# Optimization experiments

Hardware: AMD Instinct MI355X
Metric: run time of the kernel (lower is better)

Reference implementation:

```python
import jax, jax.numpy as jnp
import numpy as np

N_NODES = 8192
DIM = 512

def setup_inputs() -> dict:
    key = jax.random.key(0)
    k1, k2, k3, k4 = jax.random.split(key, 4)
    x = jax.random.normal(k1, (N_NODES, DIM), dtype=jnp.float32)
    adj = jax.random.uniform(k2, (N_NODES, N_NODES), dtype=jnp.float32)
    # nn.Linear(dim, dim): weight [out, in], bias [out]
    bound = 1.0 / np.sqrt(DIM)
    W = jax.random.uniform(k3, (DIM, DIM), minval=-bound, maxval=bound, dtype=jnp.float32)
    b = jax.random.uniform(k4, (DIM,), minval=-bound, maxval=bound, dtype=jnp.float32)
    return {"x": x, "adj": adj, "W": W, "b": b}

def reference(x, adj, W, b):
    # agg = adj @ x : [N, dim]
    agg = jnp.matmul(adj, x)
    # Linear: agg @ W.T + b, then ReLU
    out = jnp.matmul(agg, W.T) + b
    return jax.nn.relu(out)
```

## Files before the change

### kernel.cpp

```cpp
#include <hip/hip_runtime.h>
#include <stdint.h>

typedef __bf16 bf16_t;
typedef bf16_t bf16x8 __attribute__((ext_vector_type(8)));
typedef bf16_t bf16x4 __attribute__((ext_vector_type(4)));
typedef float f32x4 __attribute__((ext_vector_type(4)));

#define N_NODES 8192
#define DIM 512

typedef __attribute__((address_space(1))) void as1_void;
typedef __attribute__((address_space(3))) void as3_void;

__device__ __forceinline__ void gload_lds16(const void* g, void* l) {
  __builtin_amdgcn_global_load_lds((as1_void*)g, (as3_void*)l, 16, 0, 0);
}

__global__ __launch_bounds__(256) void k_transpose_x(const float* __restrict__ x,
                                                     bf16_t* __restrict__ xT) {
  __shared__ float tile[64][65];
  const int m0 = blockIdx.x * 64;
  const int n0 = blockIdx.y * 64;
  const int t = threadIdx.x;
  const int r = t >> 4;
  const int c = (t & 15) << 2;
#pragma unroll
  for (int i = 0; i < 4; ++i) {
    f32x4 v = *(const f32x4*)&x[(size_t)(m0 + r + i * 16) * DIM + n0 + c];
    tile[r + i * 16][c + 0] = v.x;
    tile[r + i * 16][c + 1] = v.y;
    tile[r + i * 16][c + 2] = v.z;
    tile[r + i * 16][c + 3] = v.w;
  }
  __syncthreads();
#pragma unroll
  for (int i = 0; i < 4; ++i) {
    const int rn = r + i * 16;
    bf16x4 o = {(bf16_t)tile[c + 0][rn], (bf16_t)tile[c + 1][rn],
                (bf16_t)tile[c + 2][rn], (bf16_t)tile[c + 3][rn]};
    *(bf16x4*)&xT[(size_t)(n0 + rn) * N_NODES + m0 + c] = o;
  }
}

__global__ __launch_bounds__(256) void k_cvt_w(const float* __restrict__ W,
                                               bf16_t* __restrict__ Wb) {
  const int t = blockIdx.x * 256 + threadIdx.x;
  f32x4 v = *(const f32x4*)&W[(size_t)t * 4];
  bf16x4 o = {(bf16_t)v.x, (bf16_t)v.y, (bf16_t)v.z, (bf16_t)v.w};
  *(bf16x4*)&Wb[(size_t)t * 4] = o;
}

template <int S>
__global__ __launch_bounds__(256, 3) void k_gemm1(const float* __restrict__ A,
                                                  const bf16_t* __restrict__ Bt,
                                                  float* __restrict__ P) {
  constexpr int K = N_NODES;
  constexpr int KC = K / S;
  constexpr int NIT = KC / 32;
  __shared__ float As[2][128 * 32];
  __shared__ bf16_t Bs[2][128 * 32];

  const int b = blockIdx.x;
  const int xcd = b & 7;
  const int i6 = b >> 3;
  const int n_tile = i6 & 3;
  const int s = (i6 >> 2) & (S - 1);
  const int mg = (i6 >> 2) / S;
  const int m0 = (mg * 8 + xcd) * 128;
  const int n0 = n_tile * 128;

  const int t = threadIdx.x;
  const int lane = t & 63;
  const int w = t >> 6;
  const int wr = w & 1;
  const int wc = w >> 1;
  const int lrow = lane & 15;
  const int quad = lane >> 4;

  const int aoff = ((t & 7) ^ ((t >> 3) & 7)) * 4;
  const int boff = ((t & 3) ^ ((t >> 3) & 3)) * 8;
  const float* ag = A + (size_t)(m0 + (t >> 3)) * K + (size_t)s * KC + aoff;
  const bf16_t* bg = Bt + (size_t)(n0 + (t >> 2)) * K + (size_t)s * KC + boff;

  auto stage = [&](int it, int buf) {
    const int kc = it * 32;
#pragma unroll
    for (int i = 0; i < 4; ++i)
      gload_lds16(ag + (size_t)(i * 32) * K + kc, &As[buf][(i * 256 + t) * 4]);
#pragma unroll
    for (int i = 0; i < 2; ++i)
      gload_lds16(bg + (size_t)(i * 64) * K + kc, &Bs[buf][(i * 256 + t) * 8]);
  };

  const int apc0 = ((quad * 2) ^ (lrow & 7)) * 4;
  const int apc1 = (((quad * 2) ^ (lrow & 7)) ^ 1) * 4;
  const int bpc = (quad ^ ((lrow >> 1) & 3)) * 8;

  f32x4 acc[4][4] = {};

  auto compute = [&](int buf) {
    bf16x8 af[4], bfr[4];
#pragma unroll
    for (int ii = 0; ii < 4; ++ii) {
      const int rb = (wr * 64 + ii * 16 + lrow) * 32;
      f32x4 a0 = *(const f32x4*)&As[buf][rb + apc0];
      f32x4 a1 = *(const f32x4*)&As[buf][rb + apc1];
#pragma unroll
      for (int z = 0; z < 4; ++z) {
        af[ii][z] = (bf16_t)a0[z];
        af[ii][z + 4] = (bf16_t)a1[z];
      }
    }
#pragma unroll
    for (int jj = 0; jj < 4; ++jj)
      bfr[jj] = *(const bf16x8*)&Bs[buf][(wc * 64 + jj * 16 + lrow) * 32 + bpc];
#pragma unroll
    for (int ii = 0; ii < 4; ++ii)
#pragma unroll
      for (int jj = 0; jj < 4; ++jj)
        acc[ii][jj] =
            __builtin_amdgcn_mfma_f32_16x16x32_bf16(af[ii], bfr[jj], acc[ii][jj], 0, 0, 0);
  };

  stage(0, 0);
  __syncthreads();
#pragma unroll 1
  for (int it = 0; it < NIT; it += 2) {
    stage(it + 1, 1);
    compute(0);
    __syncthreads();
    if (it + 2 < NIT) stage(it + 2, 0);
    compute(1);
    __syncthreads();
  }

  float* Pp = P + (size_t)s * N_NODES * DIM;
#pragma unroll
  for (int ii = 0; ii < 4; ++ii)
#pragma unroll
    for (int jj = 0; jj < 4; ++jj) {
      const int col = n0 + wc * 64 + jj * 16 + lrow;
#pragma unroll
      for (int r = 0; r < 4; ++r) {
        const int row = m0 + wr * 64 + ii * 16 + quad * 4 + r;
        Pp[(size_t)row * DIM + col] = acc[ii][jj][r];
      }
    }
}

template <int S>
__global__ __launch_bounds__(256, 2) void k_gemm2(const float* __restrict__ P,
                                                  const bf16_t* __restrict__ Bw,
                                                  const float* __restrict__ bias,
                                                  float* __restrict__ out) {
  constexpr int K = DIM;
  constexpr int LDA = 72;
  constexpr int LDB = 72;
  constexpr size_t PS = (size_t)N_NODES * DIM;
  __shared__ bf16_t As[64 * LDA];
  __shared__ bf16_t Bs[128 * LDB];

  const int b = blockIdx.x;
  const int xcd = b & 7;
  const int j = b >> 3;
  const int n0 = (j & 3) * 128;
  const int m0 = ((j >> 2) * 8 + xcd) * 64;
  const int t = threadIdx.x;
  const int lane = t & 63;
  const int w = t >> 6;
  const int wr = w & 1;
  const int wc = w >> 1;
  const int lrow = lane & 15;
  const int quad = lane >> 4;
  const int ar = t >> 2, aq = t & 3;
  const int br = t >> 1, bq = t & 1;

  const float* ap = P + (size_t)(m0 + ar) * K + aq * 16;
  const bf16_t* bp = Bw + (size_t)(n0 + br) * K + bq * 32;
  bf16_t* aw = &As[ar * LDA + aq * 16];
  bf16_t* bw = &Bs[br * LDB + bq * 32];

  f32x4 acc[2][4] = {};

  for (int k0 = 0; k0 < K; k0 += 64) {
    f32x4 av[4];
#pragma unroll
    for (int z = 0; z < 4; ++z) av[z] = *(const f32x4*)(ap + k0 + z * 4);
#pragma unroll
    for (int s2 = 1; s2 < S; ++s2)
#pragma unroll
      for (int z = 0; z < 4; ++z) av[z] += *(const f32x4*)(ap + s2 * PS + k0 + z * 4);
    bf16x8 b0 = *(const bf16x8*)(bp + k0);
    bf16x8 b1 = *(const bf16x8*)(bp + k0 + 8);
    bf16x8 b2 = *(const bf16x8*)(bp + k0 + 16);
    bf16x8 b3 = *(const bf16x8*)(bp + k0 + 24);
    bf16x8 a0, a1;
#pragma unroll
    for (int z = 0; z < 4; ++z) {
      a0[z] = (bf16_t)av[0][z];
      a0[z + 4] = (bf16_t)av[1][z];
      a1[z] = (bf16_t)av[2][z];
      a1[z + 4] = (bf16_t)av[3][z];
    }
    __syncthreads();
    *(bf16x8*)aw = a0;
    *(bf16x8*)(aw + 8) = a1;
    *(bf16x8*)bw = b0;
    *(bf16x8*)(bw + 8) = b1;
    *(bf16x8*)(bw + 16) = b2;
    *(bf16x8*)(bw + 24) = b3;
    __syncthreads();
#pragma unroll
    for (int kk = 0; kk < 64; kk += 32) {
      bf16x8 af0 = *(const bf16x8*)&As[(wr * 32 + 0 + lrow) * LDA + kk + quad * 8];
      bf16x8 af1 = *(const bf16x8*)&As[(wr * 32 + 16 + lrow) * LDA + kk + quad * 8];
      bf16x8 bf0 = *(const bf16x8*)&Bs[(wc * 64 + 0 + lrow) * LDB + kk + quad * 8];
      bf16x8 bf1 = *(const bf16x8*)&Bs[(wc * 64 + 16 + lrow) * LDB + kk + quad * 8];
      bf16x8 bf2 = *(const bf16x8*)&Bs[(wc * 64 + 32 + lrow) * LDB + kk + quad * 8];
      bf16x8 bf3 = *(const bf16x8*)&Bs[(wc * 64 + 48 + lrow) * LDB + kk + quad * 8];
      acc[0][0] = __builtin_amdgcn_mfma_f32_16x16x32_bf16(af0, bf0, acc[0][0], 0, 0, 0);
      acc[0][1] = __builtin_amdgcn_mfma_f32_16x16x32_bf16(af0, bf1, acc[0][1], 0, 0, 0);
      acc[0][2] = __builtin_amdgcn_mfma_f32_16x16x32_bf16(af0, bf2, acc[0][2], 0, 0, 0);
      acc[0][3] = __builtin_amdgcn_mfma_f32_16x16x32_bf16(af0, bf3, acc[0][3], 0, 0, 0);
      acc[1][0] = __builtin_amdgcn_mfma_f32_16x16x32_bf16(af1, bf0, acc[1][0], 0, 0, 0);
      acc[1][1] = __builtin_amdgcn_mfma_f32_16x16x32_bf16(af1, bf1, acc[1][1], 0, 0, 0);
      acc[1][2] = __builtin_amdgcn_mfma_f32_16x16x32_bf16(af1, bf2, acc[1][2], 0, 0, 0);
      acc[1][3] = __builtin_amdgcn_mfma_f32_16x16x32_bf16(af1, bf3, acc[1][3], 0, 0, 0);
    }
  }

#pragma unroll
  for (int i = 0; i < 2; ++i)
#pragma unroll
    for (int j2 = 0; j2 < 4; ++j2) {
      const int col = n0 + wc * 64 + j2 * 16 + lrow;
      const float bj = bias[col];
#pragma unroll
      for (int r = 0; r < 4; ++r) {
        const int row = m0 + wr * 32 + i * 16 + quad * 4 + r;
        float v = acc[i][j2][r] + bj;
        out[(size_t)row * DIM + col] = v > 0.0f ? v : 0.0f;
      }
    }
}

extern "C" void kernel_launch(void* const* d_in, const int* in_sizes, int n_in,
                              void* d_out, int out_size, void* d_ws, size_t ws_size,
                              hipStream_t stream) {
  const float* x = (const float*)d_in[0];
  const float* adj = (const float*)d_in[1];
  const float* W = (const float*)d_in[2];
  const float* b = (const float*)d_in[3];
  float* out = (float*)d_out;

  bf16_t* xT = (bf16_t*)d_ws;
  bf16_t* Wb = xT + (size_t)DIM * N_NODES;
  float* P = (float*)(Wb + (size_t)DIM * DIM);
  const size_t base = (size_t)DIM * N_NODES * 2 + (size_t)DIM * DIM * 2;
  const size_t pslab = (size_t)N_NODES * DIM * 4;

  k_transpose_x<<<dim3(N_NODES / 64, DIM / 64), 256, 0, stream>>>(x, xT);
  k_cvt_w<<<dim3((DIM * DIM / 4) / 256), 256, 0, stream>>>(W, Wb);

  if (ws_size >= base + 4 * pslab) {
    k_gemm1<4><<<dim3(256 * 4), 256, 0, stream>>>(adj, xT, P);
    k_gemm2<4><<<dim3(512), 256, 0, stream>>>(P, Wb, b, out);
  } else {
    k_gemm1<1><<<dim3(256), 256, 0, stream>>>(adj, xT, P);
    k_gemm2<1><<<dim3(512), 256, 0, stream>>>(P, Wb, b, out);
  }
}
```

Baseline: 507.0 us.

## Reassociate to adj@(xW^T) and fuse bias+ReLU into single main GEMM

Computes Y = x·W^T first in a small GEMM, writing it transposed in bf16, then runs a single large GEMM adj·Y with bias and ReLU fused in the epilogue. This removes the split-K partial-sum buffer, the second GEMM, and the separate transpose/convert kernels. The main kernel uses 64x128 tiles with a 4-buffer software pipeline and manual vmcnt waits. It rounds the intermediate Y to bf16 rather than the aggregated features, which changes the numerics slightly.

```diff
diff --git a/kernel.cpp b/kernel.cpp
--- a/kernel.cpp
+++ b/kernel.cpp
@@ -3,7 +3,6 @@
 
 typedef __bf16 bf16_t;
 typedef bf16_t bf16x8 __attribute__((ext_vector_type(8)));
-typedef bf16_t bf16x4 __attribute__((ext_vector_type(4)));
 typedef float f32x4 __attribute__((ext_vector_type(4)));
 
 #define N_NODES 8192
@@ -16,58 +15,16 @@
   __builtin_amdgcn_global_load_lds((as1_void*)g, (as3_void*)l, 16, 0, 0);
 }
 
-__global__ __launch_bounds__(256) void k_transpose_x(const float* __restrict__ x,
-                                                     bf16_t* __restrict__ xT) {
-  __shared__ float tile[64][65];
-  const int m0 = blockIdx.x * 64;
-  const int n0 = blockIdx.y * 64;
-  const int t = threadIdx.x;
-  const int r = t >> 4;
-  const int c = (t & 15) << 2;
-#pragma unroll
-  for (int i = 0; i < 4; ++i) {
-    f32x4 v = *(const f32x4*)&x[(size_t)(m0 + r + i * 16) * DIM + n0 + c];
-    tile[r + i * 16][c + 0] = v.x;
-    tile[r + i * 16][c + 1] = v.y;
-    tile[r + i * 16][c + 2] = v.z;
-    tile[r + i * 16][c + 3] = v.w;
-  }
-  __syncthreads();
-#pragma unroll
-  for (int i = 0; i < 4; ++i) {
-    const int rn = r + i * 16;
-    bf16x4 o = {(bf16_t)tile[c + 0][rn], (bf16_t)tile[c + 1][rn],
-                (bf16_t)tile[c + 2][rn], (bf16_t)tile[c + 3][rn]};
-    *(bf16x4*)&xT[(size_t)(n0 + rn) * N_NODES + m0 + c] = o;
-  }
-}
-
-__global__ __launch_bounds__(256) void k_cvt_w(const float* __restrict__ W,
-                                               bf16_t* __restrict__ Wb) {
-  const int t = blockIdx.x * 256 + threadIdx.x;
-  f32x4 v = *(const f32x4*)&W[(size_t)t * 4];
-  bf16x4 o = {(bf16_t)v.x, (bf16_t)v.y, (bf16_t)v.z, (bf16_t)v.w};
-  *(bf16x4*)&Wb[(size_t)t * 4] = o;
-}
-
-template <int S>
-__global__ __launch_bounds__(256, 3) void k_gemm1(const float* __restrict__ A,
-                                                  const bf16_t* __restrict__ Bt,
-                                                  float* __restrict__ P) {
-  constexpr int K = N_NODES;
-  constexpr int KC = K / S;
-  constexpr int NIT = KC / 32;
+__global__ __launch_bounds__(256) void k_yw(const float* __restrict__ x,
+                                            const float* __restrict__ W,
+                                            bf16_t* __restrict__ Yt) {
+  constexpr int NIT = DIM / 32;
   __shared__ float As[2][128 * 32];
-  __shared__ bf16_t Bs[2][128 * 32];
+  __shared__ float Bs[2][128 * 32];
 
   const int b = blockIdx.x;
-  const int xcd = b & 7;
-  const int i6 = b >> 3;
-  const int n_tile = i6 & 3;
-  const int s = (i6 >> 2) & (S - 1);
-  const int mg = (i6 >> 2) / S;
-  const int m0 = (mg * 8 + xcd) * 128;
-  const int n0 = n_tile * 128;
+  const int n0 = (b & 3) * 128;
+  const int k0 = (b >> 2) * 128;
 
   const int t = threadIdx.x;
   const int lane = t & 63;
@@ -77,24 +34,22 @@
   const int lrow = lane & 15;
   const int quad = lane >> 4;
 
-  const int aoff = ((t & 7) ^ ((t >> 3) & 7)) * 4;
-  const int boff = ((t & 3) ^ ((t >> 3) & 3)) * 8;
-  const float* ag = A + (size_t)(m0 + (t >> 3)) * K + (size_t)s * KC + aoff;
-  const bf16_t* bg = Bt + (size_t)(n0 + (t >> 2)) * K + (size_t)s * KC + boff;
+  const int srow = t >> 3;
+  const int aoff = ((t & 7) ^ (srow & 7)) * 4;
+  const float* ag = W + (size_t)(n0 + srow) * DIM + aoff;
+  const float* bg = x + (size_t)(k0 + srow) * DIM + aoff;
 
   auto stage = [&](int it, int buf) {
     const int kc = it * 32;
 #pragma unroll
-    for (int i = 0; i < 4; ++i)
-      gload_lds16(ag + (size_t)(i * 32) * K + kc, &As[buf][(i * 256 + t) * 4]);
-#pragma unroll
-    for (int i = 0; i < 2; ++i)
-      gload_lds16(bg + (size_t)(i * 64) * K + kc, &Bs[buf][(i * 256 + t) * 8]);
+    for (int i = 0; i < 4; ++i) {
+      gload_lds16(ag + (size_t)(i * 32) * DIM + kc, &As[buf][(i * 256 + t) * 4]);
+      gload_lds16(bg + (size_t)(i * 32) * DIM + kc, &Bs[buf][(i * 256 + t) * 4]);
+    }
   };
 
   const int apc0 = ((quad * 2) ^ (lrow & 7)) * 4;
   const int apc1 = (((quad * 2) ^ (lrow & 7)) ^ 1) * 4;
-  const int bpc = (quad ^ ((lrow >> 1) & 3)) * 8;
 
   f32x4 acc[4][4] = {};
 
@@ -112,8 +67,16 @@
       }
     }
 #pragma unroll
-    for (int jj = 0; jj < 4; ++jj)
-      bfr[jj] = *(const bf16x8*)&Bs[buf][(wc * 64 + jj * 16 + lrow) * 32 + bpc];
+    for (int jj = 0; jj < 4; ++jj) {
+      const int rb = (wc * 64 + jj * 16 + lrow) * 32;
+      f32x4 b0 = *(const f32x4*)&Bs[buf][rb + apc0];
+      f32x4 b1 = *(const f32x4*)&Bs[buf][rb + apc1];
+#pragma unroll
+      for (int z = 0; z < 4; ++z) {
+        bfr[jj][z] = (bf16_t)b0[z];
+        bfr[jj][z + 4] = (bf16_t)b1[z];
+      }
+    }
 #pragma unroll
     for (int ii = 0; ii < 4; ++ii)
 #pragma unroll
@@ -124,47 +87,45 @@
 
   stage(0, 0);
   __syncthreads();
+  int cur = 0;
 #pragma unroll 1
-  for (int it = 0; it < NIT; it += 2) {
-    stage(it + 1, 1);
-    compute(0);
+  for (int it = 0; it < NIT; ++it) {
+    if (it + 1 < NIT) stage(it + 1, cur ^ 1);
+    compute(cur);
     __syncthreads();
-    if (it + 2 < NIT) stage(it + 2, 0);
-    compute(1);
-    __syncthreads();
+    cur ^= 1;
   }
 
-  float* Pp = P + (size_t)s * N_NODES * DIM;
 #pragma unroll
   for (int ii = 0; ii < 4; ++ii)
 #pragma unroll
     for (int jj = 0; jj < 4; ++jj) {
-      const int col = n0 + wc * 64 + jj * 16 + lrow;
+      const int col = k0 + wc * 64 + jj * 16 + lrow;
 #pragma unroll
       for (int r = 0; r < 4; ++r) {
-        const int row = m0 + wr * 64 + ii * 16 + quad * 4 + r;
-        Pp[(size_t)row * DIM + col] = acc[ii][jj][r];
-      }
-    }
-}
-
-template <int S>
-__global__ __launch_bounds__(256, 2) void k_gemm2(const float* __restrict__ P,
-                                                  const bf16_t* __restrict__ Bw,
-                                                  const float* __restrict__ bias,
-                                                  float* __restrict__ out) {
-  constexpr int K = DIM;
-  constexpr int LDA = 72;
-  constexpr int LDB = 72;
-  constexpr size_t PS = (size_t)N_NODES * DIM;
-  __shared__ bf16_t As[64 * LDA];
-  __shared__ bf16_t Bs[128 * LDB];
+        const int row = n0 + wr * 64 + ii * 16 + quad * 4 + r;
+        Yt[(size_t)row * N_NODES + col] = (bf16_t)acc[ii][jj][r];
+      }
+    }
+}
+
+__global__ __launch_bounds__(256) void k_main(const float* __restrict__ A,
+                                              const bf16_t* __restrict__ Bt,
+                                              const float* __restrict__ bias,
+                                              float* __restrict__ out) {
+  constexpr int K = N_NODES;
+  constexpr int NIT = K / 32;
+  __shared__ float As[4][64 * 32];
+  __shared__ bf16_t Bs[4][128 * 32];
 
   const int b = blockIdx.x;
   const int xcd = b & 7;
-  const int j = b >> 3;
-  const int n0 = (j & 3) * 128;
-  const int m0 = ((j >> 2) * 8 + xcd) * 64;
+  const int i6 = b >> 3;
+  const int n_tile = i6 & 3;
+  const int mg = i6 >> 2;
+  const int m0 = (mg * 8 + xcd) * 64;
+  const int n0 = n_tile * 128;
+
   const int t = threadIdx.x;
   const int lane = t & 63;
   const int w = t >> 6;
@@ -172,73 +133,84 @@
   const int wc = w >> 1;
   const int lrow = lane & 15;
   const int quad = lane >> 4;
-  const int ar = t >> 2, aq = t & 3;
-  const int br = t >> 1, bq = t & 1;
-
-  const float* ap = P + (size_t)(m0 + ar) * K + aq * 16;
-  const bf16_t* bp = Bw + (size_t)(n0 + br) * K + bq * 32;
-  bf16_t* aw = &As[ar * LDA + aq * 16];
-  bf16_t* bw = &Bs[br * LDB + bq * 32];
+
+  const int aoff = ((t & 7) ^ ((t >> 3) & 7)) * 4;
+  const int boff = ((t & 3) ^ ((t >> 3) & 3)) * 8;
+  const float* ag = A + (size_t)(m0 + (t >> 3)) * K + aoff;
+  const bf16_t* bg = Bt + (size_t)(n0 + (t >> 2)) * K + boff;
+
+  auto stage = [&](int it, int buf) {
+    const int kc = it * 32;
+#pragma unroll
+    for (int i = 0; i < 2; ++i)
+      gload_lds16(ag + (size_t)(i * 32) * K + kc, &As[buf][(i * 256 + t) * 4]);
+#pragma unroll
+    for (int i = 0; i < 2; ++i)
+      gload_lds16(bg + (size_t)(i * 64) * K + kc, &Bs[buf][(i * 256 + t) * 8]);
+  };
+
+  const int apc0 = ((quad * 2) ^ (lrow & 7)) * 4;
+  const int apc1 = (((quad * 2) ^ (lrow & 7)) ^ 1) * 4;
+  const int bpc = (quad ^ ((lrow >> 1) & 3)) * 8;
 
   f32x4 acc[2][4] = {};
 
-  for (int k0 = 0; k0 < K; k0 += 64) {
-    f32x4 av[4];
-#pragma unroll
-    for (int z = 0; z < 4; ++z) av[z] = *(const f32x4*)(ap + k0 + z * 4);
-#pragma unroll
-    for (int s2 = 1; s2 < S; ++s2)
-#pragma unroll
-      for (int z = 0; z < 4; ++z) av[z] += *(const f32x4*)(ap + s2 * PS + k0 + z * 4);
-    bf16x8 b0 = *(const bf16x8*)(bp + k0);
-    bf16x8 b1 = *(const bf16x8*)(bp + k0 + 8);
-    bf16x8 b2 = *(const bf16x8*)(bp + k0 + 16);
-    bf16x8 b3 = *(const bf16x8*)(bp + k0 + 24);
-    bf16x8 a0, a1;
-#pragma unroll
-    for (int z = 0; z < 4; ++z) {
-      a0[z] = (bf16_t)av[0][z];
-      a0[z + 4] = (bf16_t)av[1][z];
-      a1[z] = (bf16_t)av[2][z];
-      a1[z + 4] = (bf16_t)av[3][z];
-    }
-    __syncthreads();
-    *(bf16x8*)aw = a0;
-    *(bf16x8*)(aw + 8) = a1;
-    *(bf16x8*)bw = b0;
-    *(bf16x8*)(bw + 8) = b1;
-    *(bf16x8*)(bw + 16) = b2;
-    *(bf16x8*)(bw + 24) = b3;
-    __syncthreads();
-#pragma unroll
-    for (int kk = 0; kk < 64; kk += 32) {
-      bf16x8 af0 = *(const bf16x8*)&As[(wr * 32 + 0 + lrow) * LDA + kk + quad * 8];
-      bf16x8 af1 = *(const bf16x8*)&As[(wr * 32 + 16 + lrow) * LDA + kk + quad * 8];
-      bf16x8 bf0 = *(const bf16x8*)&Bs[(wc * 64 + 0 + lrow) * LDB + kk + quad * 8];
-      bf16x8 bf1 = *(const bf16x8*)&Bs[(wc * 64 + 16 + lrow) * LDB + kk + quad * 8];
-      bf16x8 bf2 = *(const bf16x8*)&Bs[(wc * 64 + 32 + lrow) * LDB + kk + quad * 8];
-      bf16x8 bf3 = *(const bf16x8*)&Bs[(wc * 64 + 48 + lrow) * LDB + kk + quad * 8];
-      acc[0][0] = __builtin_amdgcn_mfma_f32_16x16x32_bf16(af0, bf0, acc[0][0], 0, 0, 0);
-      acc[0][1] = __builtin_amdgcn_mfma_f32_16x16x32_bf16(af0, bf1, acc[0][1], 0, 0, 0);
-      acc[0][2] = __builtin_amdgcn_mfma_f32_16x16x32_bf16(af0, bf2, acc[0][2], 0, 0, 0);
-      acc[0][3] = __builtin_amdgcn_mfma_f32_16x16x32_bf16(af0, bf3, acc[0][3], 0, 0, 0);
-      acc[1][0] = __builtin_amdgcn_mfma_f32_16x16x32_bf16(af1, bf0, acc[1][0], 0, 0, 0);
-      acc[1][1] = __builtin_amdgcn_mfma_f32_16x16x32_bf16(af1, bf1, acc[1][1], 0, 0, 0);
-      acc[1][2] = __builtin_amdgcn_mfma_f32_16x16x32_bf16(af1, bf2, acc[1][2], 0, 0, 0);
-      acc[1][3] = __builtin_amdgcn_mfma_f32_16x16x32_bf16(af1, bf3, acc[1][3], 0, 0, 0);
-    }
+  auto compute = [&](int buf) {
+    bf16x8 af[2], bfr[4];
+#pragma unroll
+    for (int ii = 0; ii < 2; ++ii) {
+      const int rb = (wr * 32 + ii * 16 + lrow) * 32;
+      f32x4 a0 = *(const f32x4*)&As[buf][rb + apc0];
+      f32x4 a1 = *(const f32x4*)&As[buf][rb + apc1];
+#pragma unroll
+      for (int z = 0; z < 4; ++z) {
+        af[ii][z] = (bf16_t)a0[z];
+        af[ii][z + 4] = (bf16_t)a1[z];
+      }
+    }
+#pragma unroll
+    for (int jj = 0; jj < 4; ++jj)
+      bfr[jj] = *(const bf16x8*)&Bs[buf][(wc * 64 + jj * 16 + lrow) * 32 + bpc];
+#pragma unroll
+    for (int ii = 0; ii < 2; ++ii)
+#pragma unroll
+      for (int jj = 0; jj < 4; ++jj)
+        acc[ii][jj] =
+            __builtin_amdgcn_mfma_f32_16x16x32_bf16(af[ii], bfr[jj], acc[ii][jj], 0, 0, 0);
+  };
+
+  float bjv[4];
+#pragma unroll
+  for (int jj = 0; jj < 4; ++jj) bjv[jj] = bias[n0 + wc * 64 + jj * 16 + lrow];
+
+  stage(0, 0);
+  stage(1, 1);
+  stage(2, 2);
+
+#pragma unroll 1
+  for (int it = 0; it < NIT; ++it) {
+    if (it < NIT - 2) {
+      asm volatile("s_waitcnt vmcnt(8)" ::: "memory");
+    } else if (it == NIT - 2) {
+      asm volatile("s_waitcnt vmcnt(4)" ::: "memory");
+    } else {
+      asm volatile("s_waitcnt vmcnt(0)" ::: "memory");
+    }
+    asm volatile("s_waitcnt lgkmcnt(0)" ::: "memory");
+    asm volatile("s_barrier" ::: "memory");
+    if (it + 3 < NIT) stage(it + 3, (it + 3) & 3);
+    compute(it & 3);
   }
 
 #pragma unroll
-  for (int i = 0; i < 2; ++i)
-#pragma unroll
-    for (int j2 = 0; j2 < 4; ++j2) {
-      const int col = n0 + wc * 64 + j2 * 16 + lrow;
-      const float bj = bias[col];
+  for (int ii = 0; ii < 2; ++ii)
+#pragma unroll
+    for (int jj = 0; jj < 4; ++jj) {
+      const int col = n0 + wc * 64 + jj * 16 + lrow;
 #pragma unroll
       for (int r = 0; r < 4; ++r) {
-        const int row = m0 + wr * 32 + i * 16 + quad * 4 + r;
-        float v = acc[i][j2][r] + bj;
+        const int row = m0 + wr * 32 + ii * 16 + quad * 4 + r;
+        float v = acc[ii][jj][r] + bjv[jj];
         out[(size_t)row * DIM + col] = v > 0.0f ? v : 0.0f;
       }
     }
@@ -253,20 +225,8 @@
   const float* b = (const float*)d_in[3];
   float* out = (float*)d_out;
 
-  bf16_t* xT = (bf16_t*)d_ws;
-  bf16_t* Wb = xT + (size_t)DIM * N_NODES;
-  float* P = (float*)(Wb + (size_t)DIM * DIM);
-  const size_t base = (size_t)DIM * N_NODES * 2 + (size_t)DIM * DIM * 2;
-  const size_t pslab = (size_t)N_NODES * DIM * 4;
-
-  k_transpose_x<<<dim3(N_NODES / 64, DIM / 64), 256, 0, stream>>>(x, xT);
-  k_cvt_w<<<dim3((DIM * DIM / 4) / 256), 256, 0, stream>>>(W, Wb);
-
-  if (ws_size >= base + 4 * pslab) {
-    k_gemm1<4><<<dim3(256 * 4), 256, 0, stream>>>(adj, xT, P);
-    k_gemm2<4><<<dim3(512), 256, 0, stream>>>(P, Wb, b, out);
-  } else {
-    k_gemm1<1><<<dim3(256), 256, 0, stream>>>(adj, xT, P);
-    k_gemm2<1><<<dim3(512), 256, 0, stream>>>(P, Wb, b, out);
-  }
-}
+  bf16_t* Yt = (bf16_t*)d_ws;
+
+  k_yw<<<dim3(256), 256, 0, stream>>>(x, W, Yt);
+  k_main<<<dim3(512), 256, 0, stream>>>(adj, Yt, b, out);
+}
```

Measured after the change: 581.0 us. +14.6%, slower.
